# Kernel tuning notes

Measured on AMD Instinct MI355X. Metric: run time of the kernel, lower is better.

The kernel has to match this reference:

```python
import math
import jax, jax.numpy as jnp
import numpy as np

B, T, C = 2, 2048, 1024
N_HEAD = 16
HEAD_DIM = C // N_HEAD

def setup_inputs() -> dict:
    key = jax.random.key(0)
    kx, kq, kk, kv, kp = jax.random.split(key, 5)
    s = 1.0 / math.sqrt(C)
    return {
        "x": jax.random.normal(kx, (B, T, C), dtype=jnp.float32),
        "Wq": jax.random.normal(kq, (C, C), dtype=jnp.float32) * s,
        "Wk": jax.random.normal(kk, (C, C), dtype=jnp.float32) * s,
        "Wv": jax.random.normal(kv, (C, C), dtype=jnp.float32) * s,
        "Wproj": jax.random.normal(kp, (C, C), dtype=jnp.float32) * s,
    }

def reference(x, Wq, Wk, Wv, Wproj):
    b, t, c = x.shape
    # nn.Linear(no bias): x @ W.T ; weights stored [out, in]
    def heads(w):
        return (x @ w.T).reshape(b, t, N_HEAD, HEAD_DIM).transpose(0, 2, 1, 3)  # [B,H,T,D]
    q, k, v = heads(Wq), heads(Wk), heads(Wv)
    att = jnp.einsum('bhqd,bhkd->bhqk', q, k) / math.sqrt(HEAD_DIM)  # [B,H,T,T]
    causal = jnp.tril(jnp.ones((t, t), dtype=bool))
    att = jnp.where(causal, att, -jnp.inf)
    att = jax.nn.softmax(att, axis=-1)
    y = jnp.einsum('bhqk,bhkd->bhqd', att, v)           # [B,H,T,D]
    y = y.transpose(0, 2, 1, 3).reshape(b, t, c)        # [B,T,C]
    return y @ Wproj.T
```

## Files before the change

kernel.cpp:

```cpp
#include <hip/hip_runtime.h>
#include <stdint.h>

typedef uint16_t u16;
typedef uint32_t u32;
typedef __attribute__((ext_vector_type(8))) _Float16 f16x8;
typedef __attribute__((ext_vector_type(4))) _Float16 f16x4;
typedef __attribute__((ext_vector_type(4))) float f32x4;
typedef __attribute__((ext_vector_type(2))) uint32_t u32x2;

#define NB 2
#define NT 2048
#define NC 1024
#define NH 16
#define ND 64
#define NM (NB*NT)
#define LOG2E 1.44269504088896340736f
#define PSTRIDE 4608

__device__ __forceinline__ u16 f2h(float f) {
  _Float16 h = (_Float16)f;
  return __builtin_bit_cast(u16, h);
}

__global__ __launch_bounds__(256) void cvt_kernel(const float* __restrict__ src,
                                                  u16* __restrict__ dst, int n4) {
  int i = blockIdx.x * 256 + threadIdx.x;
  if (i >= n4) return;
  float4 v = ((const float4*)src)[i];
  ushort4 o;
  o.x = f2h(v.x); o.y = f2h(v.y); o.z = f2h(v.z); o.w = f2h(v.w);
  ((ushort4*)dst)[i] = o;
}

__global__ __launch_bounds__(256) void cvtw_kernel(const float* __restrict__ w0,
                                                   const float* __restrict__ w1,
                                                   const float* __restrict__ w2,
                                                   const float* __restrict__ w3,
                                                   u16* __restrict__ dst) {
  int i = blockIdx.x * 256 + threadIdx.x;
  int which = i >> 18;
  const float* src = (which == 0) ? w0 : (which == 1) ? w1 : (which == 2) ? w2 : w3;
  int j = i & 262143;
  float4 v = ((const float4*)src)[j];
  ushort4 o;
  o.x = f2h(v.x); o.y = f2h(v.y); o.z = f2h(v.z); o.w = f2h(v.w);
  ((ushort4*)dst)[i] = o;
}

__device__ __forceinline__ void gload16(const void* g, void* l) {
  __builtin_amdgcn_global_load_lds(
      (const __attribute__((address_space(1))) void*)g,
      (__attribute__((address_space(3))) void*)l, 16, 0, 0);
}

template<int EPI>
__global__ __launch_bounds__(256) void gemm_bt(const u16* __restrict__ A,
                                               const u16* __restrict__ Bw,
                                               int K, int N,
                                               u16* __restrict__ oq, u16* __restrict__ okk,
                                               u16* __restrict__ ovt,
                                               float* __restrict__ of) {
  __shared__ __align__(16) u16 SH[4*128*64];
  u16* Al = SH;
  u16* Bl = SH + 2*128*64;
  const int tid = threadIdx.x, lane = tid & 63, wid = tid >> 6;
  const int g = lane >> 4, qq = lane & 15;
  const int wm = wid >> 1, wn = wid & 1;
  const int m0 = blockIdx.y * 128, n0 = blockIdx.x * 128;
  const int srow = lane >> 3;
  const int scol8 = (lane & 7) ^ srow;

  f32x4 acc[4][4] = {};
  const int nk = K >> 6;

  #pragma unroll
  for (int pp = 0; pp < 4; ++pp) {
    int r = wid*32 + pp*8;
    gload16(A  + (size_t)(m0 + r + srow)*K + scol8*8, &Al[r*64]);
    gload16(Bw + (size_t)(n0 + r + srow)*K + scol8*8, &Bl[r*64]);
  }

  for (int kt = 0; kt < nk; ++kt) {
    const int cur = kt & 1;
    __syncthreads();
    if (kt + 1 < nk) {
      const int k1 = (kt + 1) << 6;
      #pragma unroll
      for (int pp = 0; pp < 4; ++pp) {
        int r = wid*32 + pp*8;
        gload16(A  + (size_t)(m0 + r + srow)*K + k1 + scol8*8, &Al[(cur^1)*8192 + r*64]);
        gload16(Bw + (size_t)(n0 + r + srow)*K + k1 + scol8*8, &Bl[(cur^1)*8192 + r*64]);
      }
    }
    #pragma unroll
    for (int kk = 0; kk < 2; ++kk) {
      f16x8 af[4], bfr[4];
      #pragma unroll
      for (int mt = 0; mt < 4; ++mt) {
        int row = wm*64 + mt*16 + qq;
        af[mt] = *(const f16x8*)&Al[cur*8192 + row*64 + (((kk*4 + g) ^ (qq & 7))*8)];
      }
      #pragma unroll
      for (int nt = 0; nt < 4; ++nt) {
        int row = wn*64 + nt*16 + qq;
        bfr[nt] = *(const f16x8*)&Bl[cur*8192 + row*64 + (((kk*4 + g) ^ (qq & 7))*8)];
      }
      #pragma unroll
      for (int mt = 0; mt < 4; ++mt)
        #pragma unroll
        for (int nt = 0; nt < 4; ++nt)
          acc[mt][nt] = __builtin_amdgcn_mfma_f32_16x16x32_f16(af[mt], bfr[nt], acc[mt][nt], 0, 0, 0);
    }
  }

  if (EPI == 0) {
    __syncthreads();
    u16* reg = SH + wid*4096;
    const int sel = n0 >> 10;
    const int h = ((n0 & 1023) >> 6) + wn;
    const int bq = m0 >> 11;

    if (sel < 2) {
      const float scale = (sel == 0) ? 0.125f*LOG2E : 1.0f;
      #pragma unroll
      for (int mt = 0; mt < 4; ++mt)
        #pragma unroll
        for (int r = 0; r < 4; ++r) {
          int mloc = mt*16 + g*4 + r;
          #pragma unroll
          for (int nt = 0; nt < 4; ++nt) {
            int d = nt*16 + qq;
            reg[mloc*64 + (d ^ (g << 4))] = f2h(acc[mt][nt][r] * scale);
          }
        }
      u16* dst = (sel == 0) ? oq : okk;
      const int slot = lane & 7;
      #pragma unroll
      for (int i = 0; i < 8; ++i) {
        int row = i*8 + (lane >> 3);
        int physslot = slot ^ (((row >> 2) & 3) << 1);
        f16x8 vvv = *(const f16x8*)&reg[row*64 + physslot*8];
        int m = m0 + wm*64 + row;
        int t = m & (NT-1);
        *(f16x8*)(dst + (((size_t)(bq*NH + h)*NT + t)*ND) + slot*8) = vvv;
      }
    } else {
      #pragma unroll
      for (int nt = 0; nt < 4; ++nt) {
        int d = nt*16 + qq;
        int f = (d & 7) << 3;
        #pragma unroll
        for (int mt = 0; mt < 4; ++mt)
          #pragma unroll
          for (int rp = 0; rp < 2; ++rp) {
            int r = rp*2;
            int mloc = mt*16 + g*4 + r;
            u32 pk = (u32)f2h(acc[mt][nt][r]) | ((u32)f2h(acc[mt][nt][r+1]) << 16);
            *(u32*)&reg[d*64 + (mloc ^ f)] = pk;
          }
      }
      const int slot = lane & 7;
      const int t0 = m0 + wm*64;
      #pragma unroll
      for (int i = 0; i < 8; ++i) {
        int d = i*8 + (lane >> 3);
        int physslot = slot ^ (d & 7);
        f16x8 vvv = *(const f16x8*)&reg[d*64 + physslot*8];
        int t = (t0 & (NT-1)) + slot*8;
        *(f16x8*)(ovt + ((size_t)(bq*NH + h)*ND + d)*NT + t) = vvv;
      }
    }
  } else {
    #pragma unroll
    for (int mt = 0; mt < 4; ++mt)
      #pragma unroll
      for (int r = 0; r < 4; ++r) {
        int m = m0 + wm*64 + mt*16 + g*4 + r;
        #pragma unroll
        for (int nt = 0; nt < 4; ++nt) {
          int n = n0 + wn*64 + nt*16 + qq;
          of[(size_t)m*N + n] = acc[mt][nt][r];
        }
      }
  }
}

#define IT(q,s,c,m) ((u32)(q) | ((u32)(s)<<8) | ((u32)(c)<<16) | ((u32)(m)<<24))
__global__ __launch_bounds__(256, 5) void attn_kernel(const u16* __restrict__ q,
                                                      const u16* __restrict__ k,
                                                      const u16* __restrict__ vt,
                                                      u16* __restrict__ y,
                                                      u16* __restrict__ part) {
  static const u32 items[48] = {
    IT(15,0,16,0), IT(30,0,16,1), IT(31,0,16,1), IT(31,16,16,2),
    IT(14,0,15,0), IT(28,0,15,1), IT(29,0,15,1), IT(29,15,15,2), IT(30,16,15,2),
    IT(13,0,14,0), IT(26,0,14,1), IT(27,0,14,1), IT(27,14,14,2), IT(28,15,14,2),
    IT(12,0,13,0), IT(24,0,13,1), IT(25,0,13,1), IT(25,13,13,2), IT(26,14,13,2),
    IT(11,0,12,0), IT(22,0,12,1), IT(23,0,12,1), IT(23,12,12,2), IT(24,13,12,2),
    IT(10,0,11,0), IT(20,0,11,1), IT(21,0,11,1), IT(21,11,11,2), IT(22,12,11,2),
    IT( 9,0,10,0), IT(18,0,10,1), IT(19,0,10,1), IT(19,10,10,2), IT(20,11,10,2),
    IT( 8,0, 9,0), IT(16,0, 9,1), IT(17,0, 9,1), IT(17, 9, 9,2), IT(18,10, 9,2),
    IT( 7,0, 8,0), IT(16,9, 8,2),
    IT( 6,0, 7,0), IT( 5,0, 6,0), IT( 4,0, 5,0), IT( 3,0, 4,0),
    IT( 2,0, 3,0), IT( 1,0, 2,0), IT( 0,0, 1,0)
  };
  __shared__ __align__(16) u16 Kl[2][64*64];
  __shared__ __align__(16) u16 Vl[2][64*64];
  const int tid = threadIdx.x, lane = tid & 63, wid = tid >> 6;
  const int g = lane >> 4, qq = lane & 15;
  const int bh = blockIdx.x;
  const u32 it = items[blockIdx.y];
  const int qtile = it & 255;
  const int ks = (it >> 8) & 255;
  const int kc = (it >> 16) & 255;
  const int mode = it >> 24;
  const int qs = qtile * 64;
  const u16* qp = q  + (size_t)bh*NT*ND;
  const u16* kp = k  + (size_t)bh*NT*ND;
  const u16* vp = vt + (size_t)bh*ND*NT;
  const int b = bh >> 4, h = bh & 15;
  const int srow = lane >> 3;
  const int scol8 = (lane & 7) ^ (srow & 7);

  f16x8 aq[2];
  {
    int t = qs + wid*16 + qq;
    #pragma unroll
    for (int c = 0; c < 2; ++c)
      aq[c] = *(const f16x8*)(qp + (size_t)t*ND + c*32 + 8*g);
  }

  f16x4 ones4;
  #pragma unroll
  for (int i = 0; i < 4; ++i) ones4[i] = (_Float16)1.0f;

  f32x4 accO[4] = {};
  f32x4 accS = {};
  float m_run = -1e30f;

  #pragma unroll
  for (int pp = 0; pp < 2; ++pp) {
    int issue = wid*2 + pp;
    int row = issue*8 + srow;
    gload16(kp + (size_t)(ks*64 + row)*ND + scol8*8, &Kl[0][issue*512]);
    gload16(vp + (size_t)row*NT + ks*64 + scol8*8, &Vl[0][issue*512]);
  }

  for (int kt = ks; kt < ks + kc; ++kt) {
    const int kvs = kt*64;
    const int cur = (kt - ks) & 1;
    __syncthreads();

    if (kt + 1 < ks + kc) {
      const int kvs2 = kvs + 64;
      #pragma unroll
      for (int pp = 0; pp < 2; ++pp) {
        int issue = wid*2 + pp;
        int row = issue*8 + srow;
        gload16(kp + (size_t)(kvs2 + row)*ND + scol8*8, &Kl[cur^1][issue*512]);
        gload16(vp + (size_t)row*NT + kvs2 + scol8*8, &Vl[cur^1][issue*512]);
      }
    }

    f32x4 sacc[4] = {};
    __builtin_amdgcn_s_setprio(1);
    #pragma unroll
    for (int c = 0; c < 2; ++c) {
      #pragma unroll
      for (int nt = 0; nt < 4; ++nt) {
        int row = nt*16 + qq;
        int col = (c*32 + 8*g) ^ ((row & 7) << 3);
        f16x8 kb = *(const f16x8*)&Kl[cur][row*64 + col];
        sacc[nt] = __builtin_amdgcn_mfma_f32_16x16x32_f16(kb, aq[c], sacc[nt], 0, 0, 0);
      }
    }
    __builtin_amdgcn_s_setprio(0);

    if (kvs + 63 > qs + wid*16) {
      int qg = qs + wid*16 + qq;
      #pragma unroll
      for (int nt = 0; nt < 4; ++nt)
        #pragma unroll
        for (int r = 0; r < 4; ++r)
          if (kvs + nt*16 + g*4 + r > qg) sacc[nt][r] = -1e30f;
    }

    float m0a = fmaxf(fmaxf(sacc[0][0], sacc[0][1]), fmaxf(sacc[0][2], sacc[0][3]));
    float m1a = fmaxf(fmaxf(sacc[1][0], sacc[1][1]), fmaxf(sacc[1][2], sacc[1][3]));
    float m2a = fmaxf(fmaxf(sacc[2][0], sacc[2][1]), fmaxf(sacc[2][2], sacc[2][3]));
    float m3a = fmaxf(fmaxf(sacc[3][0], sacc[3][1]), fmaxf(sacc[3][2], sacc[3][3]));
    float mloc = fmaxf(fmaxf(m0a, m1a), fmaxf(m2a, m3a));

    const bool defer = __all(mloc <= m_run + 8.f);
    float mnew;
    if (defer) {
      mnew = m_run;
    } else {
      float mf = fmaxf(mloc, __shfl_xor(mloc, 16));
      mf = fmaxf(mf, __shfl_xor(mf, 32));
      mnew = fmaxf(m_run, mf);
      float a = exp2f(m_run - mnew);
      m_run = mnew;
      #pragma unroll
      for (int dt = 0; dt < 4; ++dt) accO[dt] *= a;
      accS *= a;
    }

    f16x4 pb[4];
    #pragma unroll
    for (int nt = 0; nt < 4; ++nt) {
      float p0 = exp2f(sacc[nt][0] - mnew);
      float p1 = exp2f(sacc[nt][1] - mnew);
      float p2 = exp2f(sacc[nt][2] - mnew);
      float p3 = exp2f(sacc[nt][3] - mnew);
      u32x2 w;
      w.x = __builtin_bit_cast(u32, __builtin_amdgcn_cvt_pkrtz(p0, p1));
      w.y = __builtin_bit_cast(u32, __builtin_amdgcn_cvt_pkrtz(p2, p3));
      pb[nt] = __builtin_bit_cast(f16x4, w);
    }

    __builtin_amdgcn_s_setprio(1);
    #pragma unroll
    for (int nt = 0; nt < 4; ++nt) {
      accS = __builtin_amdgcn_mfma_f32_16x16x16f16(ones4, pb[nt], accS, 0, 0, 0);
      #pragma unroll
      for (int dt = 0; dt < 4; ++dt) {
        int vrow = dt*16 + qq;
        int slot = (2*nt + (g >> 1)) ^ (vrow & 7);
        f16x4 vb = *(const f16x4*)&Vl[cur][vrow*64 + slot*8 + (g & 1)*4];
        accO[dt] = __builtin_amdgcn_mfma_f32_16x16x16f16(vb, pb[nt], accO[dt], 0, 0, 0);
      }
    }
    __builtin_amdgcn_s_setprio(0);
  }

  const float inv = 1.0f / accS[0];
  if (mode == 0) {
    int t = qs + wid*16 + qq;
    #pragma unroll
    for (int dt = 0; dt < 4; ++dt) {
      u32x2 st;
      st.x = (u32)f2h(accO[dt][0]*inv) | ((u32)f2h(accO[dt][1]*inv) << 16);
      st.y = (u32)f2h(accO[dt][2]*inv) | ((u32)f2h(accO[dt][3]*inv) << 16);
      *(u32x2*)(y + ((size_t)(b*NT + t))*NC + h*ND + dt*16 + g*4) = st;
    }
  } else {
    const int slot = ((bh << 4) + (qtile - 16))*2 + (mode - 1);
    u16* pp = part + (size_t)slot * PSTRIDE;
    float* hd = (float*)(pp + 4096);
    const int rloc = wid*16 + qq;
    #pragma unroll
    for (int dt = 0; dt < 4; ++dt) {
      u32x2 st;
      st.x = (u32)f2h(accO[dt][0]*inv) | ((u32)f2h(accO[dt][1]*inv) << 16);
      st.y = (u32)f2h(accO[dt][2]*inv) | ((u32)f2h(accO[dt][3]*inv) << 16);
      *(u32x2*)(pp + rloc*64 + dt*16 + g*4) = st;
    }
    if (g == 0) { hd[rloc] = m_run; hd[64 + rloc] = accS[0]; }
  }
}

__global__ __launch_bounds__(256) void combine_kernel(const u16* __restrict__ part,
                                                      u16* __restrict__ y) {
  const int jj = blockIdx.x;
  const int bh = blockIdx.y;
  const int b = bh >> 4, h = bh & 15;
  const u16* p0 = part + (size_t)(((bh << 4) + jj)*2) * PSTRIDE;
  const u16* p1 = p0 + PSTRIDE;
  const float* h0 = (const float*)(p0 + 4096);
  const float* h1 = (const float*)(p1 + 4096);
  const int tid = threadIdx.x;
  const int d0 = (tid & 7) * 8;
  #pragma unroll
  for (int i = 0; i < 2; ++i) {
    int r = (tid >> 3) + 32*i;
    float m1 = h0[r], l1 = h0[64 + r];
    float m2 = h1[r], l2 = h1[64 + r];
    float mm = fmaxf(m1, m2);
    float w1 = exp2f(m1 - mm) * l1, w2 = exp2f(m2 - mm) * l2;
    float inv = 1.0f / (w1 + w2);
    float a1 = w1 * inv, a2 = w2 * inv;
    f16x8 o1 = *(const f16x8*)&p0[r*64 + d0];
    f16x8 o2 = *(const f16x8*)&p1[r*64 + d0];
    f16x8 out;
    #pragma unroll
    for (int e = 0; e < 8; ++e)
      out[e] = (_Float16)(a1 * (float)o1[e] + a2 * (float)o2[e]);
    int t = (16 + jj)*64 + r;
    *(f16x8*)(y + ((size_t)(b*NT + t))*NC + h*ND + d0) = out;
  }
}

extern "C" void kernel_launch(void* const* d_in, const int* in_sizes, int n_in,
                              void* d_out, int out_size, void* d_ws, size_t ws_size,
                              hipStream_t stream) {
  const float* x  = (const float*)d_in[0];
  const float* Wq = (const float*)d_in[1];
  const float* Wk = (const float*)d_in[2];
  const float* Wv = (const float*)d_in[3];
  const float* Wp = (const float*)d_in[4];

  u16* xb   = (u16*)d_ws;
  u16* wqkv = xb   + (size_t)NM*NC;
  u16* wpj  = wqkv + (size_t)3*NC*NC;
  u16* qb   = wpj  + (size_t)NC*NC;
  u16* kb   = qb   + (size_t)NM*NC;
  u16* vtb  = kb   + (size_t)NM*NC;
  u16* yb   = vtb  + (size_t)NM*NC;
  u16* part = xb;
  size_t need = ((size_t)NM*NC*5 + (size_t)4*NC*NC) * sizeof(u16);
  if (ws_size < need) return;

  cvt_kernel<<<NM*NC/4/256, 256, 0, stream>>>(x, xb, NM*NC/4);
  cvtw_kernel<<<4*NC*NC/4/256, 256, 0, stream>>>(Wq, Wk, Wv, Wp, wqkv);

  gemm_bt<0><<<dim3(3*NC/128, NM/128), 256, 0, stream>>>(xb, wqkv, NC, 3*NC,
                                                         qb, kb, vtb, nullptr);
  attn_kernel<<<dim3(NB*NH, 48), 256, 0, stream>>>(qb, kb, vtb, yb, part);
  combine_kernel<<<dim3(16, NB*NH), 256, 0, stream>>>(part, yb);
  gemm_bt<1><<<dim3(NC/128, NM/128), 256, 0, stream>>>(yb, wpj, NC, NC,
                                                       nullptr, nullptr, nullptr,
                                                       (float*)d_out);
}
```

Before: 113.7 us.

## Rebalance causal attention split-KV schedule with finer chunks and three-way combine

Replaces the 48-item work list with 60 items that cap each block at 12 K-tiles instead of 16, splitting longer query tiles into two or three KV chunks. The combine kernel now merges two or three partials per tile over 20 query tiles, and the partial slot layout is re-indexed per head with a tighter stride. The aim is to shorten the longest block and cut tail imbalance in the attention grid. In exchange there are more partial writes and more combine work.

```diff
diff --git a/kernel.cpp b/kernel.cpp
--- a/kernel.cpp
+++ b/kernel.cpp
@@ -15,7 +15,7 @@
 #define ND 64
 #define NM (NB*NT)
 #define LOG2E 1.44269504088896340736f
-#define PSTRIDE 4608
+#define PSTRIDE 4352
 
 __device__ __forceinline__ u16 f2h(float f) {
   _Float16 h = (_Float16)f;
@@ -191,18 +191,24 @@
                                                       const u16* __restrict__ vt,
                                                       u16* __restrict__ y,
                                                       u16* __restrict__ part) {
-  static const u32 items[48] = {
-    IT(15,0,16,0), IT(30,0,16,1), IT(31,0,16,1), IT(31,16,16,2),
-    IT(14,0,15,0), IT(28,0,15,1), IT(29,0,15,1), IT(29,15,15,2), IT(30,16,15,2),
-    IT(13,0,14,0), IT(26,0,14,1), IT(27,0,14,1), IT(27,14,14,2), IT(28,15,14,2),
-    IT(12,0,13,0), IT(24,0,13,1), IT(25,0,13,1), IT(25,13,13,2), IT(26,14,13,2),
-    IT(11,0,12,0), IT(22,0,12,1), IT(23,0,12,1), IT(23,12,12,2), IT(24,13,12,2),
-    IT(10,0,11,0), IT(20,0,11,1), IT(21,0,11,1), IT(21,11,11,2), IT(22,12,11,2),
-    IT( 9,0,10,0), IT(18,0,10,1), IT(19,0,10,1), IT(19,10,10,2), IT(20,11,10,2),
-    IT( 8,0, 9,0), IT(16,0, 9,1), IT(17,0, 9,1), IT(17, 9, 9,2), IT(18,10, 9,2),
-    IT( 7,0, 8,0), IT(16,9, 8,2),
-    IT( 6,0, 7,0), IT( 5,0, 6,0), IT( 4,0, 5,0), IT( 3,0, 4,0),
-    IT( 2,0, 3,0), IT( 1,0, 2,0), IT( 0,0, 1,0)
+  static const u32 items[60] = {
+    IT(11,0,12,0),  IT(22,0,12,21), IT(23,0,12,23), IT(23,12,12,24),
+    IT(10,0,11,0),  IT(20,0,11,17), IT(21,0,11,19), IT(21,11,11,20),
+    IT(22,12,11,22),IT(30,0,11,43), IT(31,0,11,46), IT(31,11,11,47),
+    IT(9,0,10,0),   IT(18,0,10,13), IT(19,0,10,15), IT(19,10,10,16),
+    IT(20,11,10,18),IT(27,0,10,34), IT(28,0,10,37), IT(28,10,10,38),
+    IT(29,0,10,40), IT(29,10,10,41),IT(29,20,10,42),IT(30,11,10,44),
+    IT(30,21,10,45),IT(31,22,10,48),
+    IT(8,0,9,0),    IT(16,0,9,9),   IT(17,0,9,11),  IT(17,9,9,12),
+    IT(18,10,9,14), IT(24,0,9,25),  IT(25,0,9,28),  IT(25,9,9,29),
+    IT(26,0,9,31),  IT(26,9,9,32),  IT(26,18,9,33), IT(27,10,9,35),
+    IT(27,19,9,36), IT(28,20,9,39),
+    IT(7,0,8,0),    IT(14,0,8,5),   IT(15,0,8,7),   IT(15,8,8,8),
+    IT(16,9,8,10),  IT(24,9,8,26),  IT(24,17,8,27), IT(25,18,8,30),
+    IT(6,0,7,0),    IT(12,0,7,1),   IT(13,0,7,3),   IT(13,7,7,4),
+    IT(14,8,7,6),
+    IT(5,0,6,0),    IT(12,7,6,2),
+    IT(4,0,5,0), IT(3,0,4,0), IT(2,0,3,0), IT(1,0,2,0), IT(0,0,1,0)
   };
   __shared__ __align__(16) u16 Kl[2][64*64];
   __shared__ __align__(16) u16 Vl[2][64*64];
@@ -345,7 +351,7 @@
       *(u32x2*)(y + ((size_t)(b*NT + t))*NC + h*ND + dt*16 + g*4) = st;
     }
   } else {
-    const int slot = ((bh << 4) + (qtile - 16))*2 + (mode - 1);
+    const int slot = bh*48 + (mode - 1);
     u16* pp = part + (size_t)slot * PSTRIDE;
     float* hd = (float*)(pp + 4096);
     const int rloc = wid*16 + qq;
@@ -362,31 +368,37 @@
 
 __global__ __launch_bounds__(256) void combine_kernel(const u16* __restrict__ part,
                                                       u16* __restrict__ y) {
-  const int jj = blockIdx.x;
+  const int qtile = 12 + blockIdx.x;
   const int bh = blockIdx.y;
   const int b = bh >> 4, h = bh & 15;
-  const u16* p0 = part + (size_t)(((bh << 4) + jj)*2) * PSTRIDE;
-  const u16* p1 = p0 + PSTRIDE;
-  const float* h0 = (const float*)(p0 + 4096);
-  const float* h1 = (const float*)(p1 + 4096);
+  const int nc = (qtile < 24) ? 2 : 3;
+  const int pbase = (qtile < 24) ? (qtile - 12)*2 : 24 + (qtile - 24)*3;
+  const u16* p0 = part + (size_t)(bh*48 + pbase) * PSTRIDE;
   const int tid = threadIdx.x;
   const int d0 = (tid & 7) * 8;
   #pragma unroll
   for (int i = 0; i < 2; ++i) {
     int r = (tid >> 3) + 32*i;
-    float m1 = h0[r], l1 = h0[64 + r];
-    float m2 = h1[r], l2 = h1[64 + r];
-    float mm = fmaxf(m1, m2);
-    float w1 = exp2f(m1 - mm) * l1, w2 = exp2f(m2 - mm) * l2;
-    float inv = 1.0f / (w1 + w2);
-    float a1 = w1 * inv, a2 = w2 * inv;
-    f16x8 o1 = *(const f16x8*)&p0[r*64 + d0];
-    f16x8 o2 = *(const f16x8*)&p1[r*64 + d0];
+    float m0 = ((const float*)(p0 + 4096))[r];
+    float l0 = ((const float*)(p0 + 4096))[64 + r];
+    float m1 = ((const float*)(p0 + PSTRIDE + 4096))[r];
+    float l1 = ((const float*)(p0 + PSTRIDE + 4096))[64 + r];
+    float m2 = (nc == 3) ? ((const float*)(p0 + 2*PSTRIDE + 4096))[r]      : -1e30f;
+    float l2 = (nc == 3) ? ((const float*)(p0 + 2*PSTRIDE + 4096))[64 + r] : 0.f;
+    float mm = fmaxf(fmaxf(m0, m1), m2);
+    float w0 = exp2f(m0 - mm) * l0;
+    float w1 = exp2f(m1 - mm) * l1;
+    float w2 = exp2f(m2 - mm) * l2;
+    float inv = 1.0f / (w0 + w1 + w2);
+    float a0 = w0 * inv, a1 = w1 * inv, a2 = w2 * inv;
+    f16x8 o0 = *(const f16x8*)&p0[r*64 + d0];
+    f16x8 o1 = *(const f16x8*)&p0[PSTRIDE + r*64 + d0];
+    f16x8 o2 = *(const f16x8*)&p0[2*PSTRIDE + r*64 + d0];
     f16x8 out;
     #pragma unroll
     for (int e = 0; e < 8; ++e)
-      out[e] = (_Float16)(a1 * (float)o1[e] + a2 * (float)o2[e]);
-    int t = (16 + jj)*64 + r;
+      out[e] = (_Float16)(a0*(float)o0[e] + a1*(float)o1[e] + a2*(float)o2[e]);
+    int t = qtile*64 + r;
     *(f16x8*)(y + ((size_t)(b*NT + t))*NC + h*ND + d0) = out;
   }
 }
@@ -416,8 +428,8 @@
 
   gemm_bt<0><<<dim3(3*NC/128, NM/128), 256, 0, stream>>>(xb, wqkv, NC, 3*NC,
                                                          qb, kb, vtb, nullptr);
-  attn_kernel<<<dim3(NB*NH, 48), 256, 0, stream>>>(qb, kb, vtb, yb, part);
-  combine_kernel<<<dim3(16, NB*NH), 256, 0, stream>>>(part, yb);
+  attn_kernel<<<dim3(NB*NH, 60), 256, 0, stream>>>(qb, kb, vtb, yb, part);
+  combine_kernel<<<dim3(20, NB*NH), 256, 0, stream>>>(part, yb);
   gemm_bt<1><<<dim3(NC/128, NM/128), 256, 0, stream>>>(yb, wpj, NC, NC,
                                                        nullptr, nullptr, nullptr,
                                                        (float*)d_out);
```

Measured after the change: 112.0 us. Within noise of the previous version (-1.5%).
